# Kernel optimization log

Hardware: AMD Instinct MI355X
Metric: run time of the kernel (lower is better)

Reference implementation:

```python
import jax, jax.numpy as jnp
import numpy as np

N_NODES = 10000
N_EDGES = 160000
G = 64  # num graphs in batch
D_IN, D_HID, D_OUT = 1280, 512, 256
EPS = 1e-12


def setup_inputs() -> dict:
    key = jax.random.key(0)
    ks = jax.random.split(key, 16)
    x = jax.random.normal(ks[0], (N_NODES, D_IN), dtype=jnp.float32)
    edge_index = jax.random.randint(ks[1], (2, N_EDGES), 0, N_NODES, dtype=jnp.int64)
    batch = jnp.sort(jax.random.randint(ks[2], (N_NODES,), 0, G, dtype=jnp.int64))
    vector = jax.random.normal(ks[3], (G, D_OUT), dtype=jnp.float32)
    s = 0.02
    p = {
        'W1': jax.random.normal(ks[4], (D_IN, D_HID), dtype=jnp.float32) * s,
        'b1': jnp.zeros((D_HID,), jnp.float32),
        'W2': jax.random.normal(ks[5], (D_HID, D_HID), dtype=jnp.float32) * s,
        'b2': jnp.zeros((D_HID,), jnp.float32),
        'W3': jax.random.normal(ks[6], (D_HID, D_HID), dtype=jnp.float32) * s,
        'b3': jnp.zeros((D_HID,), jnp.float32),
        'W4': jax.random.normal(ks[7], (D_HID, D_OUT), dtype=jnp.float32) * s,
        'b4': jnp.zeros((D_OUT,), jnp.float32),
        'cW1': jax.random.normal(ks[8], (512, 256), dtype=jnp.float32) * s,
        'cb1': jnp.zeros((256,), jnp.float32),
        'cW2': jax.random.normal(ks[9], (256, 64), dtype=jnp.float32) * s,
        'cb2': jnp.zeros((64,), jnp.float32),
        'cW3': jax.random.normal(ks[10], (64, 1), dtype=jnp.float32) * s,
        'cb3': jnp.zeros((1,), jnp.float32),
    }
    return dict(x=x, edge_index=edge_index, batch=batch, vector=vector, **p)


def _gcn_conv(h, W, b, src, dst, norm):
    # PyG GCNConv: X W, then symmetric-normalized scatter-add over edges (self-loops included)
    h = h @ W
    msg = h[src] * norm[:, None]              # [E+N, d]
    out = jax.ops.segment_sum(msg, dst, num_segments=N_NODES)
    return out + b


def reference(x, edge_index, batch, vector,
              W1, b1, W2, b2, W3, b3, W4, b4,
              cW1, cb1, cW2, cb2, cW3, cb3):
    loops = jnp.arange(N_NODES, dtype=edge_index.dtype)
    src = jnp.concatenate([edge_index[0], loops])
    dst = jnp.concatenate([edge_index[1], loops])
    deg = jax.ops.segment_sum(jnp.ones_like(dst, dtype=x.dtype), dst, num_segments=N_NODES)
    dis = deg ** -0.5                          # deg >= 1 due to self loops
    norm = dis[src] * dis[dst]

    h = _gcn_conv(x, W1, b1, src, dst, norm)
    h = jax.nn.relu(h)                          # dropout is identity in eval
    h = _gcn_conv(h, W2, b2, src, dst, norm)
    h = jax.nn.relu(h)
    h = _gcn_conv(h, W3, b3, src, dst, norm)
    h = jax.nn.relu(h)
    h = _gcn_conv(h, W4, b4, src, dst, norm)

    # global_mean_pool
    sums = jax.ops.segment_sum(h, batch, num_segments=G)
    cnts = jax.ops.segment_sum(jnp.ones((N_NODES,), h.dtype), batch, num_segments=G)
    pool = sums / jnp.maximum(cnts, 1.0)[:, None]
    # F.normalize(dim=1)
    pool = pool / jnp.maximum(jnp.linalg.norm(pool, axis=1, keepdims=True), EPS)

    combined = jnp.concatenate([pool, vector], axis=1)   # [G, 512]
    z = jax.nn.relu(combined @ cW1 + cb1)
    z = jax.nn.relu(z @ cW2 + cb2)
    return jax.nn.sigmoid(z @ cW3 + cb3)                  # [G, 1]
```

## Files before the change

### kernel.cpp

```cpp
#include <hip/hip_runtime.h>
#include <hip/hip_bf16.h>


#define N_NODES 10000
#define N_EDGES 160000
#define NGRAPH  64
#define MPAD    10112
#define PCHUNK  16

typedef __attribute__((ext_vector_type(8))) short short8;
typedef __attribute__((ext_vector_type(4))) float f32x4;
typedef __attribute__((ext_vector_type(4))) unsigned short u16x4;

__device__ __forceinline__ unsigned short f2bf(float f) {
    unsigned u = __float_as_uint(f);
    return (unsigned short)((u + 0x7FFFu + ((u >> 16) & 1u)) >> 16);
}
__device__ __forceinline__ float bf2f(unsigned short u) {
    return __uint_as_float(((unsigned)u) << 16);
}
__device__ __forceinline__ void gl_lds16(const void* g, void* l) {
    __builtin_amdgcn_global_load_lds(
        (const __attribute__((address_space(1))) unsigned*)g,
        (__attribute__((address_space(3))) unsigned*)l, 16, 0, 0);
}

__global__ __launch_bounds__(256) void zero_i32(int* p, int n) {
    int i = blockIdx.x * 256 + threadIdx.x;
    if (i < n) p[i] = 0;
}
__global__ __launch_bounds__(256) void zero_f32(float* p, int n) {
    int i = blockIdx.x * 256 + threadIdx.x;
    if (i < n) p[i] = 0.0f;
}

__global__ __launch_bounds__(256) void conv_bf16(const float4* __restrict__ in,
                                                 u16x4* __restrict__ out, int n4) {
    int i = blockIdx.x * 256 + threadIdx.x;
    if (i >= n4) return;
    float4 v = in[i];
    u16x4 o;
    o.x = f2bf(v.x); o.y = f2bf(v.y); o.z = f2bf(v.z); o.w = f2bf(v.w);
    out[i] = o;
}

__global__ __launch_bounds__(256) void conv_transpose_w(const float* __restrict__ W,
                                                        unsigned short* __restrict__ Wt,
                                                        int K, int N) {
    __shared__ float t[32][33];
    int k0 = blockIdx.x * 32, n0 = blockIdx.y * 32;
    int tx = threadIdx.x & 31, ty = threadIdx.x >> 5;
#pragma unroll
    for (int i = 0; i < 4; i++)
        t[ty + i * 8][tx] = W[(size_t)(k0 + ty + i * 8) * N + n0 + tx];
    __syncthreads();
#pragma unroll
    for (int i = 0; i < 4; i++)
        Wt[(size_t)(n0 + ty + i * 8) * K + k0 + tx] = f2bf(t[tx][ty + i * 8]);
}

__global__ __launch_bounds__(256) void transpose_f32(const float* __restrict__ W,
                                                     float* __restrict__ Wt,
                                                     int K, int N) {
    __shared__ float t[32][33];
    int k0 = blockIdx.x * 32, n0 = blockIdx.y * 32;
    int tx = threadIdx.x & 31, ty = threadIdx.x >> 5;
#pragma unroll
    for (int i = 0; i < 4; i++)
        t[ty + i * 8][tx] = W[(size_t)(k0 + ty + i * 8) * N + n0 + tx];
    __syncthreads();
#pragma unroll
    for (int i = 0; i < 4; i++)
        Wt[(size_t)(n0 + ty + i * 8) * K + k0 + tx] = t[tx][ty + i * 8];
}

__global__ __launch_bounds__(256) void deg_count(const int* __restrict__ dst, int* __restrict__ degc, int E) {
    int e = blockIdx.x * 256 + threadIdx.x;
    if (e < E) atomicAdd(&degc[dst[e]], 1);
}
__global__ __launch_bounds__(256) void deg_fin(const int* __restrict__ degc, float* __restrict__ dis, int n) {
    int i = blockIdx.x * 256 + threadIdx.x;
    if (i < n) dis[i] = 1.0f / sqrtf((float)(degc[i] + 1));
}
__global__ __launch_bounds__(1024) void scan_offsets(const int* __restrict__ cnt,
                                                     int* __restrict__ off, int n) {
    __shared__ int buf[1024];
    __shared__ int carry;
    int t = threadIdx.x;
    if (t == 0) { carry = 0; off[0] = 0; }
    __syncthreads();
    for (int base = 0; base < n; base += 1024) {
        int v = (base + t < n) ? cnt[base + t] : 0;
        buf[t] = v;
        __syncthreads();
#pragma unroll
        for (int o = 1; o < 1024; o <<= 1) {
            int add = (t >= o) ? buf[t - o] : 0;
            __syncthreads();
            buf[t] += add;
            __syncthreads();
        }
        if (base + t < n) off[base + t + 1] = buf[t] + carry;
        __syncthreads();
        if (t == 0) carry += buf[1023];
        __syncthreads();
    }
}
__global__ __launch_bounds__(256) void csr_fill(const int* __restrict__ srcI,
                                                const int* __restrict__ dstI,
                                                const int* __restrict__ off,
                                                int* __restrict__ fc,
                                                const float* __restrict__ dis,
                                                int* __restrict__ csr_src,
                                                float* __restrict__ csr_w, int E) {
    int e = blockIdx.x * 256 + threadIdx.x;
    if (e >= E) return;
    int d = dstI[e];
    int s = srcI[e];
    int pos = off[d] + atomicAdd(&fc[d], 1);
    csr_src[pos] = s;
    csr_w[pos] = dis[s];
}

__global__ __launch_bounds__(256) void gemm_bf16(const unsigned short* __restrict__ A,
                                                 const unsigned short* __restrict__ Bt,
                                                 unsigned short* __restrict__ C,
                                                 int K, int N) {
    __shared__ short lA[64 * 64];
    __shared__ short lB[128 * 64];
    int tid = threadIdx.x;
    int lane = tid & 63;
    int wave = tid >> 6;
    int rm = blockIdx.y, cn = blockIdx.x;
    int wr = wave >> 1, wc = wave & 1;

    f32x4 acc[2][4];
#pragma unroll
    for (int m = 0; m < 2; m++)
#pragma unroll
        for (int n = 0; n < 4; n++) acc[m][n] = (f32x4){0.f, 0.f, 0.f, 0.f};

    int lrow = lane >> 3;
    int lcs = ((lane & 7) ^ (lrow & 7)) * 8;

    for (int k0 = 0; k0 < K; k0 += 64) {
        __syncthreads();
#pragma unroll
        for (int i = 0; i < 2; i++) {
            int s = wave * 2 + i;
            int row = rm * 64 + s * 8 + lrow;
            if (row > N_NODES - 1) row = N_NODES - 1;
            gl_lds16(A + (size_t)row * K + k0 + lcs, &lA[s * 512]);
        }
#pragma unroll
        for (int i = 0; i < 4; i++) {
            int s = wave * 4 + i;
            int row = cn * 128 + s * 8 + lrow;
            gl_lds16(Bt + (size_t)row * K + k0 + lcs, &lB[s * 512]);
        }
        __syncthreads();
#pragma unroll
        for (int kk = 0; kk < 64; kk += 32) {
            int cbase = (kk >> 3) + (lane >> 4);
            short8 a[2], b[4];
#pragma unroll
            for (int m = 0; m < 2; m++) {
                int r = wr * 32 + m * 16 + (lane & 15);
                a[m] = *(const short8*)&lA[r * 64 + (cbase ^ (r & 7)) * 8];
            }
#pragma unroll
            for (int n = 0; n < 4; n++) {
                int r = wc * 64 + n * 16 + (lane & 15);
                b[n] = *(const short8*)&lB[r * 64 + (cbase ^ (r & 7)) * 8];
            }
#pragma unroll
            for (int m = 0; m < 2; m++)
#pragma unroll
                for (int n = 0; n < 4; n++)
                    acc[m][n] = __builtin_amdgcn_mfma_f32_16x16x32_bf16(a[m], b[n], acc[m][n], 0, 0, 0);
        }
    }
    int r0 = rm * 64 + wr * 32 + (lane >> 4) * 4;
    int c0 = cn * 128 + wc * 64 + (lane & 15);
#pragma unroll
    for (int m = 0; m < 2; m++)
#pragma unroll
        for (int n = 0; n < 4; n++)
#pragma unroll
            for (int j = 0; j < 4; j++)
                C[(size_t)(r0 + m * 16 + j) * N + c0 + n * 16] = f2bf(acc[m][n][j]);
}

template<int D, bool RELU, bool OUTBF>
__global__ __launch_bounds__(D / 4) void gather_nodes(const unsigned short* __restrict__ h,
                                                      const int* __restrict__ off,
                                                      const int* __restrict__ csr_src,
                                                      const float* __restrict__ csr_w,
                                                      const float* __restrict__ dis,
                                                      const float4* __restrict__ bias,
                                                      void* __restrict__ outp) {
    int n = blockIdx.x;
    int f = threadIdx.x;
    float dn = dis[n];
    u16x4 hv = ((const u16x4*)(h + (size_t)n * D))[f];
    float ax = dn * bf2f(hv.x), ay = dn * bf2f(hv.y), az = dn * bf2f(hv.z), aw = dn * bf2f(hv.w);
    int kb = off[n], ke = off[n + 1];
    for (int k = kb; k < ke; k++) {
        int s = csr_src[k];
        float w = csr_w[k];
        u16x4 v = ((const u16x4*)(h + (size_t)s * D))[f];
        ax += w * bf2f(v.x); ay += w * bf2f(v.y); az += w * bf2f(v.z); aw += w * bf2f(v.w);
    }
    float4 bb = bias[f];
    float ox = ax * dn + bb.x, oy = ay * dn + bb.y, oz = az * dn + bb.z, ow = aw * dn + bb.w;
    if (RELU) {
        ox = fmaxf(ox, 0.f); oy = fmaxf(oy, 0.f); oz = fmaxf(oz, 0.f); ow = fmaxf(ow, 0.f);
    }
    if (OUTBF) {
        u16x4 o; o.x = f2bf(ox); o.y = f2bf(oy); o.z = f2bf(oz); o.w = f2bf(ow);
        ((u16x4*)outp)[(size_t)n * (D / 4) + f] = o;
    } else {
        ((float4*)outp)[(size_t)n * (D / 4) + f] = make_float4(ox, oy, oz, ow);
    }
}

__global__ __launch_bounds__(256) void pool_partial(const float* __restrict__ agg,
                                                    const int* __restrict__ batch,
                                                    float* __restrict__ pool) {
    int c0 = blockIdx.x * PCHUNK;
    int t = threadIdx.x;
    int end = c0 + PCHUNK;
    if (end > N_NODES) end = N_NODES;
    float acc = 0.0f;
    int cur = batch[c0];
    for (int n = c0; n < end; n++) {
        int g = batch[n];
        if (g != cur) {
            atomicAdd(&pool[cur * 256 + t], acc);
            acc = 0.0f;
            cur = g;
        }
        acc += agg[(size_t)n * 256 + t];
    }
    atomicAdd(&pool[cur * 256 + t], acc);
}

__device__ __forceinline__ int lbound(const int* __restrict__ a, int n, int key) {
    int lo = 0, hi = n;
    while (lo < hi) {
        int mid = (lo + hi) >> 1;
        if (a[mid] < key) lo = mid + 1; else hi = mid;
    }
    return lo;
}

__global__ __launch_bounds__(256) void head_comb(const float* __restrict__ pool,
                                                 const int* __restrict__ batch,
                                                 const float* __restrict__ vec,
                                                 float* __restrict__ comb) {
    int g = blockIdx.x;
    int t = threadIdx.x;
    __shared__ float red[4];
    int lo = lbound(batch, N_NODES, g);
    int hi = lbound(batch, N_NODES, g + 1);
    float c = fmaxf((float)(hi - lo), 1.0f);
    float pm = pool[g * 256 + t] / c;

    float ss = pm * pm;
#pragma unroll
    for (int o = 32; o; o >>= 1) ss += __shfl_down(ss, o);
    if ((t & 63) == 0) red[t >> 6] = ss;
    __syncthreads();
    if (t == 0) {
        float tot = red[0] + red[1] + red[2] + red[3];
        red[0] = 1.0f / fmaxf(sqrtf(tot), 1e-12f);
    }
    __syncthreads();
    comb[g * 512 + t] = pm * red[0];
    comb[g * 512 + 256 + t] = vec[g * 256 + t];
}

__global__ __launch_bounds__(256) void head_z1(const float* __restrict__ comb,
                                               const float* __restrict__ cW1t,
                                               const float* __restrict__ cb1,
                                               float* __restrict__ z1) {
    int wid = (blockIdx.x * 256 + threadIdx.x) >> 6;
    int lane = threadIdx.x & 63;
    int g = wid >> 8;
    int o = wid & 255;
    const float4* ca = (const float4*)(comb + g * 512);
    const float4* wa = (const float4*)(cW1t + (size_t)o * 512);
    float s = 0.0f;
#pragma unroll
    for (int r = 0; r < 2; r++) {
        float4 c4 = ca[lane * 2 + r];
        float4 w4 = wa[lane * 2 + r];
        s += c4.x * w4.x + c4.y * w4.y + c4.z * w4.z + c4.w * w4.w;
    }
#pragma unroll
    for (int off = 32; off; off >>= 1) s += __shfl_down(s, off);
    if (lane == 0) z1[g * 256 + o] = fmaxf(s + cb1[o], 0.0f);
}

__global__ __launch_bounds__(256) void head_z2z3(const float* __restrict__ z1,
                                                 const float* __restrict__ cW2t,
                                                 const float* __restrict__ cb2,
                                                 const float* __restrict__ cW3,
                                                 const float* __restrict__ cb3,
                                                 float* __restrict__ out) {
    int g = blockIdx.x;
    int t = threadIdx.x;
    int j = t >> 2;
    int q = t & 3;
    __shared__ float part[256];
    __shared__ float z2s[64];
    const float* z = z1 + g * 256;
    const float* w = cW2t + (size_t)j * 256;
    float s = 0.0f;
#pragma unroll
    for (int i = q * 64; i < q * 64 + 64; i += 4) {
        float4 zv = *(const float4*)(z + i);
        float4 wv = *(const float4*)(w + i);
        s += zv.x * wv.x + zv.y * wv.y + zv.z * wv.z + zv.w * wv.w;
    }
    part[t] = s;
    __syncthreads();
    if (q == 0) {
        float v = part[j * 4] + part[j * 4 + 1] + part[j * 4 + 2] + part[j * 4 + 3] + cb2[j];
        z2s[j] = fmaxf(v, 0.0f);
    }
    __syncthreads();
    if (t < 64) {
        float p = z2s[t] * cW3[t];
#pragma unroll
        for (int off = 32; off; off >>= 1) p += __shfl_down(p, off);
        if (t == 0) out[g] = 1.0f / (1.0f + expf(-(p + cb3[0])));
    }
}

extern "C" void kernel_launch(void* const* d_in, const int* in_sizes, int n_in,
                              void* d_out, int out_size, void* d_ws, size_t ws_size,
                              hipStream_t stream) {
    const float* x   = (const float*)d_in[0];
    const int*   ei  = (const int*)d_in[1];
    const int*   bat = (const int*)d_in[2];
    const float* vec = (const float*)d_in[3];
    const float* W1 = (const float*)d_in[4];
    const float* b1 = (const float*)d_in[5];
    const float* W2 = (const float*)d_in[6];
    const float* b2 = (const float*)d_in[7];
    const float* W3 = (const float*)d_in[8];
    const float* b3 = (const float*)d_in[9];
    const float* W4 = (const float*)d_in[10];
    const float* b4 = (const float*)d_in[11];
    const float* cW1 = (const float*)d_in[12];
    const float* cb1 = (const float*)d_in[13];
    const float* cW2 = (const float*)d_in[14];
    const float* cb2 = (const float*)d_in[15];
    const float* cW3 = (const float*)d_in[16];
    const float* cb3 = (const float*)d_in[17];

    const int* srcI = ei;
    const int* dstI = ei + N_EDGES;

    char* base = (char*)d_ws;
    float* dis      = (float*)base;            base += N_NODES * 4;
    int*   degc     = (int*)base;              base += N_NODES * 4;
    int*   off      = (int*)base;              base += (N_NODES + 1) * 4;
    int*   fc       = (int*)base;              base += N_NODES * 4 + 4;
    int*   csr_src  = (int*)base;              base += N_EDGES * 4;
    float* csr_w    = (float*)base;            base += N_EDGES * 4;
    float* pool     = (float*)base;            base += NGRAPH * 256 * 4;
    float* comb     = (float*)base;            base += NGRAPH * 512 * 4;
    float* z1       = (float*)base;            base += NGRAPH * 256 * 4;
    float* cW1t     = (float*)base;            base += 512 * 256 * 4;
    float* cW2t     = (float*)base;            base += 256 * 64 * 4;
    unsigned short* xb   = (unsigned short*)base;  base += (size_t)N_NODES * 1280 * 2;
    unsigned short* W1t  = (unsigned short*)base;  base += 512 * 1280 * 2;
    unsigned short* W2t  = (unsigned short*)base;  base += 512 * 512 * 2;
    unsigned short* W3t  = (unsigned short*)base;  base += 512 * 512 * 2;
    unsigned short* W4t  = (unsigned short*)base;  base += 256 * 512 * 2;
    unsigned short* h    = (unsigned short*)base;  base += (size_t)MPAD * 512 * 2;
    unsigned short* aggb = (unsigned short*)base;  base += (size_t)N_NODES * 512 * 2;
    float* agg4 = (float*)xb;

    conv_bf16<<<(N_NODES * 1280 / 4 + 255) / 256, 256, 0, stream>>>((const float4*)x, (u16x4*)xb, N_NODES * 1280 / 4);
    conv_transpose_w<<<dim3(1280 / 32, 512 / 32), 256, 0, stream>>>(W1, W1t, 1280, 512);
    conv_transpose_w<<<dim3(512 / 32, 512 / 32), 256, 0, stream>>>(W2, W2t, 512, 512);
    conv_transpose_w<<<dim3(512 / 32, 512 / 32), 256, 0, stream>>>(W3, W3t, 512, 512);
    conv_transpose_w<<<dim3(512 / 32, 256 / 32), 256, 0, stream>>>(W4, W4t, 512, 256);
    transpose_f32<<<dim3(512 / 32, 256 / 32), 256, 0, stream>>>(cW1, cW1t, 512, 256);
    transpose_f32<<<dim3(256 / 32, 64 / 32), 256, 0, stream>>>(cW2, cW2t, 256, 64);

    zero_i32<<<(N_NODES + 255) / 256, 256, 0, stream>>>(degc, N_NODES);
    zero_i32<<<(N_NODES + 255) / 256, 256, 0, stream>>>(fc, N_NODES);
    deg_count<<<(N_EDGES + 255) / 256, 256, 0, stream>>>(dstI, degc, N_EDGES);
    deg_fin<<<(N_NODES + 255) / 256, 256, 0, stream>>>(degc, dis, N_NODES);
    scan_offsets<<<1, 1024, 0, stream>>>(degc, off, N_NODES);
    csr_fill<<<(N_EDGES + 255) / 256, 256, 0, stream>>>(srcI, dstI, off, fc, dis, csr_src, csr_w, N_EDGES);

    gemm_bf16<<<dim3(512 / 128, MPAD / 64), 256, 0, stream>>>(xb, W1t, h, 1280, 512);
    gather_nodes<512, true, true><<<N_NODES, 128, 0, stream>>>(h, off, csr_src, csr_w, dis,
                                                               (const float4*)b1, aggb);
    gemm_bf16<<<dim3(512 / 128, MPAD / 64), 256, 0, stream>>>(aggb, W2t, h, 512, 512);
    gather_nodes<512, true, true><<<N_NODES, 128, 0, stream>>>(h, off, csr_src, csr_w, dis,
                                                               (const float4*)b2, aggb);
    gemm_bf16<<<dim3(512 / 128, MPAD / 64), 256, 0, stream>>>(aggb, W3t, h, 512, 512);
    gather_nodes<512, true, true><<<N_NODES, 128, 0, stream>>>(h, off, csr_src, csr_w, dis,
                                                               (const float4*)b3, aggb);
    gemm_bf16<<<dim3(256 / 128, MPAD / 64), 256, 0, stream>>>(aggb, W4t, h, 512, 256);
    gather_nodes<256, false, false><<<N_NODES, 64, 0, stream>>>(h, off, csr_src, csr_w, dis,
                                                                (const float4*)b4, agg4);

    zero_f32<<<(NGRAPH * 256 + 255) / 256, 256, 0, stream>>>(pool, NGRAPH * 256);
    pool_partial<<<(N_NODES + PCHUNK - 1) / PCHUNK, 256, 0, stream>>>(agg4, bat, pool);
    head_comb<<<NGRAPH, 256, 0, stream>>>(pool, bat, vec, comb);
    head_z1<<<4096, 256, 0, stream>>>(comb, cW1t, cb1, z1);
    head_z2z3<<<NGRAPH, 256, 0, stream>>>(z1, cW2t, cb2, cW3, cb3, (float*)d_out);
}
```

Baseline: 399.5 us.

## Restructure gather to one wavefront per node, fuse setup launches and scan

The neighbour-aggregation kernel now maps one 64-lane wavefront to each node, four nodes per 256-thread block, with 8 or 4 bf16 features per lane and a 4-way unrolled edge loop. This increases memory-level parallelism in the gather and cuts the number of tiny blocks. The weight-transpose launches are merged into two multi-matrix launches using blockIdx.z. The two zeroing kernels become one by making the degree and fill-count buffers adjacent. deg_fin is folded into a shuffle-based scan that also computes the inverse square roots. The changes aim to cut launch overhead and improve gather throughput; the unrolled edge loop uses more registers.

```diff
diff --git a/kernel.cpp b/kernel.cpp
--- a/kernel.cpp
+++ b/kernel.cpp
@@ -1,5 +1,6 @@
 #include <hip/hip_runtime.h>
 #include <hip/hip_bf16.h>
+#include <type_traits>
 
 
 #define N_NODES 10000
@@ -11,6 +12,7 @@
 typedef __attribute__((ext_vector_type(8))) short short8;
 typedef __attribute__((ext_vector_type(4))) float f32x4;
 typedef __attribute__((ext_vector_type(4))) unsigned short u16x4;
+typedef __attribute__((ext_vector_type(8))) unsigned short u16x8;
 
 __device__ __forceinline__ unsigned short f2bf(float f) {
     unsigned u = __float_as_uint(f);
@@ -44,11 +46,21 @@
     out[i] = o;
 }
 
-__global__ __launch_bounds__(256) void conv_transpose_w(const float* __restrict__ W,
-                                                        unsigned short* __restrict__ Wt,
-                                                        int K, int N) {
+__global__ __launch_bounds__(256) void conv_transpose_w4(
+        const float* __restrict__ W1, const float* __restrict__ W2,
+        const float* __restrict__ W3, const float* __restrict__ W4,
+        unsigned short* __restrict__ W1t, unsigned short* __restrict__ W2t,
+        unsigned short* __restrict__ W3t, unsigned short* __restrict__ W4t) {
+    const float* W; unsigned short* Wt; int K, N;
+    switch (blockIdx.z) {
+        case 0:  W = W1; Wt = W1t; K = 1280; N = 512; break;
+        case 1:  W = W2; Wt = W2t; K = 512;  N = 512; break;
+        case 2:  W = W3; Wt = W3t; K = 512;  N = 512; break;
+        default: W = W4; Wt = W4t; K = 512;  N = 256; break;
+    }
+    int k0 = blockIdx.x * 32, n0 = blockIdx.y * 32;
+    if (k0 >= K || n0 >= N) return;
     __shared__ float t[32][33];
-    int k0 = blockIdx.x * 32, n0 = blockIdx.y * 32;
     int tx = threadIdx.x & 31, ty = threadIdx.x >> 5;
 #pragma unroll
     for (int i = 0; i < 4; i++)
@@ -59,11 +71,15 @@
         Wt[(size_t)(n0 + ty + i * 8) * K + k0 + tx] = f2bf(t[tx][ty + i * 8]);
 }
 
-__global__ __launch_bounds__(256) void transpose_f32(const float* __restrict__ W,
-                                                     float* __restrict__ Wt,
-                                                     int K, int N) {
+__global__ __launch_bounds__(256) void transpose_f32_2(
+        const float* __restrict__ cW1, const float* __restrict__ cW2,
+        float* __restrict__ cW1t, float* __restrict__ cW2t) {
+    const float* W; float* Wt; int K, N;
+    if (blockIdx.z == 0) { W = cW1; Wt = cW1t; K = 512; N = 256; }
+    else                 { W = cW2; Wt = cW2t; K = 256; N = 64; }
+    int k0 = blockIdx.x * 32, n0 = blockIdx.y * 32;
+    if (k0 >= K || n0 >= N) return;
     __shared__ float t[32][33];
-    int k0 = blockIdx.x * 32, n0 = blockIdx.y * 32;
     int tx = threadIdx.x & 31, ty = threadIdx.x >> 5;
 #pragma unroll
     for (int i = 0; i < 4; i++)
@@ -78,34 +94,46 @@
     int e = blockIdx.x * 256 + threadIdx.x;
     if (e < E) atomicAdd(&degc[dst[e]], 1);
 }
-__global__ __launch_bounds__(256) void deg_fin(const int* __restrict__ degc, float* __restrict__ dis, int n) {
-    int i = blockIdx.x * 256 + threadIdx.x;
-    if (i < n) dis[i] = 1.0f / sqrtf((float)(degc[i] + 1));
-}
+
 __global__ __launch_bounds__(1024) void scan_offsets(const int* __restrict__ cnt,
-                                                     int* __restrict__ off, int n) {
-    __shared__ int buf[1024];
+                                                     int* __restrict__ off,
+                                                     float* __restrict__ dis, int n) {
+    __shared__ int wsum[16];
     __shared__ int carry;
     int t = threadIdx.x;
+    int wv = t >> 6, ln = t & 63;
     if (t == 0) { carry = 0; off[0] = 0; }
     __syncthreads();
     for (int base = 0; base < n; base += 1024) {
-        int v = (base + t < n) ? cnt[base + t] : 0;
-        buf[t] = v;
-        __syncthreads();
-#pragma unroll
-        for (int o = 1; o < 1024; o <<= 1) {
-            int add = (t >= o) ? buf[t - o] : 0;
-            __syncthreads();
-            buf[t] += add;
-            __syncthreads();
-        }
-        if (base + t < n) off[base + t + 1] = buf[t] + carry;
-        __syncthreads();
-        if (t == 0) carry += buf[1023];
-        __syncthreads();
-    }
-}
+        int idx = base + t;
+        int v = (idx < n) ? cnt[idx] : 0;
+        if (idx < n) dis[idx] = rsqrtf((float)(v + 1));
+#pragma unroll
+        for (int o = 1; o < 64; o <<= 1) {
+            int u = __shfl_up(v, o);
+            if (ln >= o) v += u;
+        }
+        if (ln == 63) wsum[wv] = v;
+        __syncthreads();
+        if (wv == 0 && ln < 16) {
+            int s = wsum[ln];
+#pragma unroll
+            for (int o = 1; o < 16; o <<= 1) {
+                int u = __shfl_up(s, o);
+                if (ln >= o) s += u;
+            }
+            wsum[ln] = s;
+        }
+        __syncthreads();
+        int add = (wv > 0) ? wsum[wv - 1] : 0;
+        int total = wsum[15];
+        if (idx < n) off[idx + 1] = v + add + carry;
+        __syncthreads();
+        if (t == 0) carry += total;
+        __syncthreads();
+    }
+}
+
 __global__ __launch_bounds__(256) void csr_fill(const int* __restrict__ srcI,
                                                 const int* __restrict__ dstI,
                                                 const int* __restrict__ off,
@@ -192,35 +220,60 @@
 }
 
 template<int D, bool RELU, bool OUTBF>
-__global__ __launch_bounds__(D / 4) void gather_nodes(const unsigned short* __restrict__ h,
-                                                      const int* __restrict__ off,
-                                                      const int* __restrict__ csr_src,
-                                                      const float* __restrict__ csr_w,
-                                                      const float* __restrict__ dis,
-                                                      const float4* __restrict__ bias,
-                                                      void* __restrict__ outp) {
-    int n = blockIdx.x;
-    int f = threadIdx.x;
+__global__ __launch_bounds__(256) void gather_nodes(const unsigned short* __restrict__ h,
+                                                    const int* __restrict__ off,
+                                                    const int* __restrict__ csr_src,
+                                                    const float* __restrict__ csr_w,
+                                                    const float* __restrict__ dis,
+                                                    const float* __restrict__ bias,
+                                                    void* __restrict__ outp) {
+    constexpr int VPL = D / 64;
+    using uvec = typename std::conditional<VPL == 8, u16x8, u16x4>::type;
+    int n = blockIdx.x * 4 + (threadIdx.x >> 6);
+    if (n >= N_NODES) return;
+    int lane = threadIdx.x & 63;
+    const unsigned short* hl = h + (size_t)lane * VPL;
     float dn = dis[n];
-    u16x4 hv = ((const u16x4*)(h + (size_t)n * D))[f];
-    float ax = dn * bf2f(hv.x), ay = dn * bf2f(hv.y), az = dn * bf2f(hv.z), aw = dn * bf2f(hv.w);
+    float acc[VPL];
+    uvec sv = *(const uvec*)(hl + (size_t)n * D);
+#pragma unroll
+    for (int j = 0; j < VPL; j++) acc[j] = dn * bf2f(sv[j]);
     int kb = off[n], ke = off[n + 1];
-    for (int k = kb; k < ke; k++) {
+    int k = kb;
+    for (; k + 4 <= ke; k += 4) {
+        int s0 = csr_src[k + 0], s1 = csr_src[k + 1], s2 = csr_src[k + 2], s3 = csr_src[k + 3];
+        float w0 = csr_w[k + 0], w1 = csr_w[k + 1], w2 = csr_w[k + 2], w3 = csr_w[k + 3];
+        uvec v0 = *(const uvec*)(hl + (size_t)s0 * D);
+        uvec v1 = *(const uvec*)(hl + (size_t)s1 * D);
+        uvec v2 = *(const uvec*)(hl + (size_t)s2 * D);
+        uvec v3 = *(const uvec*)(hl + (size_t)s3 * D);
+#pragma unroll
+        for (int j = 0; j < VPL; j++)
+            acc[j] += w0 * bf2f(v0[j]) + w1 * bf2f(v1[j]) + w2 * bf2f(v2[j]) + w3 * bf2f(v3[j]);
+    }
+    for (; k < ke; k++) {
         int s = csr_src[k];
         float w = csr_w[k];
-        u16x4 v = ((const u16x4*)(h + (size_t)s * D))[f];
-        ax += w * bf2f(v.x); ay += w * bf2f(v.y); az += w * bf2f(v.z); aw += w * bf2f(v.w);
-    }
-    float4 bb = bias[f];
-    float ox = ax * dn + bb.x, oy = ay * dn + bb.y, oz = az * dn + bb.z, ow = aw * dn + bb.w;
-    if (RELU) {
-        ox = fmaxf(ox, 0.f); oy = fmaxf(oy, 0.f); oz = fmaxf(oz, 0.f); ow = fmaxf(ow, 0.f);
+        uvec v = *(const uvec*)(hl + (size_t)s * D);
+#pragma unroll
+        for (int j = 0; j < VPL; j++) acc[j] += w * bf2f(v[j]);
+    }
+#pragma unroll
+    for (int j = 0; j < VPL; j++) {
+        float o = acc[j] * dn + bias[lane * VPL + j];
+        if (RELU) o = fmaxf(o, 0.0f);
+        acc[j] = o;
     }
     if (OUTBF) {
-        u16x4 o; o.x = f2bf(ox); o.y = f2bf(oy); o.z = f2bf(oz); o.w = f2bf(ow);
-        ((u16x4*)outp)[(size_t)n * (D / 4) + f] = o;
+        uvec ov;
+#pragma unroll
+        for (int j = 0; j < VPL; j++) ov[j] = f2bf(acc[j]);
+        *(uvec*)((unsigned short*)outp + (size_t)n * D + lane * VPL) = ov;
     } else {
-        ((float4*)outp)[(size_t)n * (D / 4) + f] = make_float4(ox, oy, oz, ow);
+#pragma unroll
+        for (int j = 0; j < VPL; j += 4)
+            *(float4*)((float*)outp + (size_t)n * D + lane * VPL + j) =
+                make_float4(acc[j], acc[j + 1], acc[j + 2], acc[j + 3]);
     }
 }
 
@@ -364,10 +417,10 @@
     const int* dstI = ei + N_EDGES;
 
     char* base = (char*)d_ws;
+    int*   degc     = (int*)base;              base += N_NODES * 4;
+    int*   fc       = (int*)base;              base += N_NODES * 4;
+    int*   off      = (int*)base;              base += (N_NODES + 1) * 4 + 4;
     float* dis      = (float*)base;            base += N_NODES * 4;
-    int*   degc     = (int*)base;              base += N_NODES * 4;
-    int*   off      = (int*)base;              base += (N_NODES + 1) * 4;
-    int*   fc       = (int*)base;              base += N_NODES * 4 + 4;
     int*   csr_src  = (int*)base;              base += N_EDGES * 4;
     float* csr_w    = (float*)base;            base += N_EDGES * 4;
     float* pool     = (float*)base;            base += NGRAPH * 256 * 4;
@@ -385,32 +438,22 @@
     float* agg4 = (float*)xb;
 
     conv_bf16<<<(N_NODES * 1280 / 4 + 255) / 256, 256, 0, stream>>>((const float4*)x, (u16x4*)xb, N_NODES * 1280 / 4);
-    conv_transpose_w<<<dim3(1280 / 32, 512 / 32), 256, 0, stream>>>(W1, W1t, 1280, 512);
-    conv_transpose_w<<<dim3(512 / 32, 512 / 32), 256, 0, stream>>>(W2, W2t, 512, 512);
-    conv_transpose_w<<<dim3(512 / 32, 512 / 32), 256, 0, stream>>>(W3, W3t, 512, 512);
-    conv_transpose_w<<<dim3(512 / 32, 256 / 32), 256, 0, stream>>>(W4, W4t, 512, 256);
-    transpose_f32<<<dim3(512 / 32, 256 / 32), 256, 0, stream>>>(cW1, cW1t, 512, 256);
-    transpose_f32<<<dim3(256 / 32, 64 / 32), 256, 0, stream>>>(cW2, cW2t, 256, 64);
-
-    zero_i32<<<(N_NODES + 255) / 256, 256, 0, stream>>>(degc, N_NODES);
-    zero_i32<<<(N_NODES + 255) / 256, 256, 0, stream>>>(fc, N_NODES);
+    conv_transpose_w4<<<dim3(40, 16, 4), 256, 0, stream>>>(W1, W2, W3, W4, W1t, W2t, W3t, W4t);
+    transpose_f32_2<<<dim3(16, 8, 2), 256, 0, stream>>>(cW1, cW2, cW1t, cW2t);
+
+    zero_i32<<<(2 * N_NODES + 255) / 256, 256, 0, stream>>>(degc, 2 * N_NODES);
     deg_count<<<(N_EDGES + 255) / 256, 256, 0, stream>>>(dstI, degc, N_EDGES);
-    deg_fin<<<(N_NODES + 255) / 256, 256, 0, stream>>>(degc, dis, N_NODES);
-    scan_offsets<<<1, 1024, 0, stream>>>(degc, off, N_NODES);
+    scan_offsets<<<1, 1024, 0, stream>>>(degc, off, dis, N_NODES);
     csr_fill<<<(N_EDGES + 255) / 256, 256, 0, stream>>>(srcI, dstI, off, fc, dis, csr_src, csr_w, N_EDGES);
 
     gemm_bf16<<<dim3(512 / 128, MPAD / 64), 256, 0, stream>>>(xb, W1t, h, 1280, 512);
-    gather_nodes<512, true, true><<<N_NODES, 128, 0, stream>>>(h, off, csr_src, csr_w, dis,
-                                                               (const float4*)b1, aggb);
+    gather_nodes<512, true, true><<<2500, 256, 0, stream>>>(h, off, csr_src, csr_w, dis, b1, aggb);
     gemm_bf16<<<dim3(512 / 128, MPAD / 64), 256, 0, stream>>>(aggb, W2t, h, 512, 512);
-    gather_nodes<512, true, true><<<N_NODES, 128, 0, stream>>>(h, off, csr_src, csr_w, dis,
-                                                               (const float4*)b2, aggb);
+    gather_nodes<512, true, true><<<2500, 256, 0, stream>>>(h, off, csr_src, csr_w, dis, b2, aggb);
     gemm_bf16<<<dim3(512 / 128, MPAD / 64), 256, 0, stream>>>(aggb, W3t, h, 512, 512);
-    gather_nodes<512, true, true><<<N_NODES, 128, 0, stream>>>(h, off, csr_src, csr_w, dis,
-                                                               (const float4*)b3, aggb);
+    gather_nodes<512, true, true><<<2500, 256, 0, stream>>>(h, off, csr_src, csr_w, dis, b3, aggb);
     gemm_bf16<<<dim3(256 / 128, MPAD / 64), 256, 0, stream>>>(aggb, W4t, h, 512, 256);
-    gather_nodes<256, false, false><<<N_NODES, 64, 0, stream>>>(h, off, csr_src, csr_w, dis,
-                                                                (const float4*)b4, agg4);
+    gather_nodes<256, false, false><<<2500, 256, 0, stream>>>(h, off, csr_src, csr_w, dis, b4, agg4);
 
     zero_f32<<<(NGRAPH * 256 + 255) / 256, 256, 0, stream>>>(pool, NGRAPH * 256);
     pool_partial<<<(N_NODES + PCHUNK - 1) / PCHUNK, 256, 0, stream>>>(agg4, bat, pool);
```

After: 356.6 us. -10.7%, faster.
